# Kernel optimization log

Measured on AMD Instinct MI355X. Metric: run time of the kernel, lower is better.

## Reference

```python
import jax, jax.numpy as jnp
import numpy as np

NUM_USERS = 100000
NUM_MOVIES = 50000
NUM_NODES = NUM_USERS + NUM_MOVIES
EMB_DIM = 64
N_LAYERS = 3
N_EDGES = 4000000


def setup_inputs() -> dict:
    key = jax.random.key(0)
    k_e, k_w = jax.random.split(key)
    edge_index = jax.random.randint(k_e, (2, N_EDGES), 0, NUM_NODES, dtype=jnp.int64 if jax.config.jax_enable_x64 else jnp.int32)
    emb_weight = jax.random.normal(k_w, (NUM_NODES, EMB_DIM), dtype=jnp.float32)
    return {"edge_index": edge_index, "emb_weight": emb_weight}


def reference(edge_index, emb_weight):
    row, col = edge_index[0], edge_index[1]
    num_nodes = emb_weight.shape[0]
    # degree of each node as a scatter-add destination (col)
    deg = jax.ops.segment_sum(jnp.ones_like(col, dtype=emb_weight.dtype), col,
                              num_segments=num_nodes)
    deg_inv_sqrt = jnp.where(deg > 0, jax.lax.rsqrt(jnp.maximum(deg, 1.0)), 0.0)
    deg_inv_sqrt = jnp.where(deg > 0, deg ** -0.5, 0.0)
    norm = deg_inv_sqrt[row] * deg_inv_sqrt[col]  # [E]

    embs = emb_weight
    acc = emb_weight  # running sum for the final mean over layers
    for _ in range(N_LAYERS):
        msgs = norm[:, None] * embs[row]  # [E, D] gather + scale
        embs = jax.ops.segment_sum(msgs, col, num_segments=num_nodes)  # [N, D]
        acc = acc + embs
    return acc / (N_LAYERS + 1)
```

## Files before the change

### kernel.cpp

```cpp
#include <hip/hip_runtime.h>
#include <hip/hip_fp16.h>

#define D 64
constexpr int TPB = 256;
constexpr int PTPB = 1024;
constexpr int CTPB = 1024;
constexpr int VSHIFT = 8;
constexpr int VNODES = 1 << VSHIFT;
constexpr int CHUNK = 16384;
constexpr int CAP = 8192;
constexpr int MAXBUK = 640;
constexpr int GPAD = 16;
typedef unsigned short u16;

__device__ inline unsigned h2pack(float a, float b) {
    unsigned lo = __half_as_ushort(__float2half_rn(a));
    unsigned hi = __half_as_ushort(__float2half_rn(b));
    return lo | (hi << 16);
}

__global__ void fuseAB_kernel(const int* __restrict__ row, const int* __restrict__ col,
                              int* __restrict__ gcnt, unsigned* __restrict__ tmp,
                              int E, int NBUK) {
    __shared__ unsigned s_stage[CHUNK];
    __shared__ int h[MAXBUK];
    __shared__ int s[1024];
    __shared__ int gbase[MAXBUK];
    int t = threadIdx.x, blk = blockIdx.x;
    for (int b = t; b < MAXBUK; b += PTPB) h[b] = 0;
    __syncthreads();
    int base = blk * CHUNK;
    int n = min(CHUNK, E - base);
    for (int i = t; i < n; i += PTPB)
        atomicAdd(&h[col[base + i] >> VSHIFT], 1);
    __syncthreads();
    int v = (t < NBUK) ? h[t] : 0;
    if (t < NBUK && v > 0) gbase[t] = atomicAdd(&gcnt[t * GPAD], v);
    s[t] = v;
    __syncthreads();
    for (int off = 1; off < 1024; off <<= 1) {
        int x = (t >= off) ? s[t - off] : 0;
        __syncthreads();
        s[t] += x;
        __syncthreads();
    }
    s[t] -= v;
    __syncthreads();
    for (int i = t; i < n; i += PTPB) {
        int c = col[base + i];
        int b = c >> VSHIFT;
        int p = atomicAdd(&s[b], 1);
        s_stage[p] = ((unsigned)(c & (VNODES - 1)) << 18) | (unsigned)row[base + i];
    }
    __syncthreads();
    int w = t >> 6, lane = t & 63;
    for (int b = w; b < NBUK; b += (PTPB >> 6)) {
        int cnt = h[b];
        if (cnt == 0) continue;
        int lo = s[b] - cnt;
        int gb = gbase[b];
        unsigned* __restrict__ dst = tmp + (size_t)b * CAP;
        for (int j = lane; j < cnt; j += 64) {
            int p = gb + j;
            if (p < CAP)
                dst[p] = s_stage[lo + j];
        }
    }
}

__global__ void bscan_kernel(const int* __restrict__ gcnt, int* __restrict__ bExcl, int nb) {
    __shared__ int s[1024];
    int t = threadIdx.x;
    int v = (t < nb) ? gcnt[t * GPAD] : 0;
    s[t] = v;
    __syncthreads();
    for (int off = 1; off < 1024; off <<= 1) {
        int x = (t >= off) ? s[t - off] : 0;
        __syncthreads();
        s[t] += x;
        __syncthreads();
    }
    if (t < nb) bExcl[t] = s[t] - v;
}

__global__ void passC_kernel(const unsigned* __restrict__ tmp, const int* __restrict__ gcnt,
                             const int* __restrict__ bExcl,
                             int* __restrict__ row_ptr, float* __restrict__ dis,
                             int* __restrict__ srow,
                             const float2* __restrict__ emb2, unsigned* __restrict__ A,
                             int N, int E) {
    __shared__ int cnt[VNODES], sc[VNODES], cur[VNODES];
    int b = blockIdx.x, t = threadIdx.x;
    int nodeBase = b << VSHIFT;
    if (t < VNODES) cnt[t] = 0;
    if (b == 0 && t < 32) A[(size_t)N * 32 + t] = 0;
    __syncthreads();
    int m = min(gcnt[b * GPAD], CAP);
    const unsigned* __restrict__ tb = tmp + (size_t)b * CAP;
    for (int i = t; i < m; i += CTPB)
        atomicAdd(&cnt[tb[i] >> 18], 1);
    __syncthreads();
    if (t < VNODES) sc[t] = cnt[t];
    __syncthreads();
    for (int off = 1; off < VNODES; off <<= 1) {
        int i = (t + 1) * (off << 1) - 1;
        if (i < VNODES) sc[i] += sc[i - off];
        __syncthreads();
    }
    if (t == 0) sc[VNODES - 1] = 0;
    __syncthreads();
    for (int off = VNODES / 2; off >= 1; off >>= 1) {
        int i = (t + 1) * (off << 1) - 1;
        if (i < VNODES) { int x = sc[i - off]; sc[i - off] = sc[i]; sc[i] += x; }
        __syncthreads();
    }
    int gbase = bExcl[b];
    if (t < VNODES) {
        int rp = gbase + sc[t];
        cur[t] = rp;
        int node = nodeBase + t;
        if (node < N) {
            row_ptr[node] = rp;
            int d = cnt[t];
            dis[node] = (d > 0) ? rsqrtf((float)d) : 0.0f;
        }
    }
    if (b == 0 && t == 0) row_ptr[N] = E;
    __syncthreads();
    for (int i = t; i < m; i += CTPB) {
        unsigned pk = tb[i];
        int p = atomicAdd(&cur[pk >> 18], 1);
        srow[p] = (int)(pk & 0x3FFFFu);
    }
    for (int i = t; i < (VNODES << 5); i += CTPB) {
        int k = i >> 5;
        int node = nodeBase + k;
        if (node < N) {
            int d = cnt[k];
            float dv = (d > 0) ? rsqrtf((float)d) : 0.0f;
            size_t o = (size_t)node * 32 + (i & 31);
            float2 x = emb2[o];
            A[o] = h2pack(dv * x.x, dv * x.y);
        }
    }
}

#define ACC8(u) do { \
    a0 += __half2float(__ushort_as_half((u16)((u).x & 0xffff))); \
    a1 += __half2float(__ushort_as_half((u16)((u).x >> 16)));    \
    a2 += __half2float(__ushort_as_half((u16)((u).y & 0xffff))); \
    a3 += __half2float(__ushort_as_half((u16)((u).y >> 16)));    \
    a4 += __half2float(__ushort_as_half((u16)((u).z & 0xffff))); \
    a5 += __half2float(__ushort_as_half((u16)((u).z >> 16)));    \
    a6 += __half2float(__ushort_as_half((u16)((u).w & 0xffff))); \
    a7 += __half2float(__ushort_as_half((u16)((u).w >> 16)));    \
} while (0)

template <int MODE, bool WRITE_DST>
__global__ void spmm_kernel(const int* __restrict__ row_ptr, const int* __restrict__ srow,
                            const float* __restrict__ dis,
                            const unsigned* __restrict__ src, unsigned* __restrict__ dst,
                            float2* __restrict__ out2, const float2* __restrict__ emb2,
                            int N) {
    if (WRITE_DST && blockIdx.x == 0 && threadIdx.x < 32)
        dst[(size_t)N * 32 + threadIdx.x] = 0;
    int wave = (blockIdx.x * blockDim.x + threadIdx.x) >> 6;
    int lane = threadIdx.x & 63;
    int half = lane >> 5;
    int sub  = lane & 31;
    int node = 2 * wave + half;
    if (node >= N) return;
    int start = row_ptr[node];
    int end   = row_ptr[node + 1];
    int hb = half << 5;
    int rg = sub >> 3;
    int q  = sub & 7;
    const uint4* __restrict__ s4 = (const uint4*)src;
    float a0 = 0, a1 = 0, a2 = 0, a3 = 0, a4 = 0, a5 = 0, a6 = 0, a7 = 0;
    for (int base = start; base < end; base += 32) {
        int mye = base + sub;
        int rr = (mye < end) ? srow[mye] : 0;
        int cnt = end - base;
        int r0 = __shfl(rr, hb +  0 + rg);
        int r1 = __shfl(rr, hb +  4 + rg);
        int r2 = __shfl(rr, hb +  8 + rg);
        int r3 = __shfl(rr, hb + 12 + rg);
        int r4 = __shfl(rr, hb + 16 + rg);
        int r5 = __shfl(rr, hb + 20 + rg);
        int r6 = __shfl(rr, hb + 24 + rg);
        int r7 = __shfl(rr, hb + 28 + rg);
        r0 = ( 0 + rg < cnt) ? r0 : N;
        r1 = ( 4 + rg < cnt) ? r1 : N;
        r2 = ( 8 + rg < cnt) ? r2 : N;
        r3 = (12 + rg < cnt) ? r3 : N;
        r4 = (16 + rg < cnt) ? r4 : N;
        r5 = (20 + rg < cnt) ? r5 : N;
        r6 = (24 + rg < cnt) ? r6 : N;
        r7 = (28 + rg < cnt) ? r7 : N;
        uint4 u0 = s4[(size_t)r0 * 8 + q];
        uint4 u1 = s4[(size_t)r1 * 8 + q];
        uint4 u2 = s4[(size_t)r2 * 8 + q];
        uint4 u3 = s4[(size_t)r3 * 8 + q];
        uint4 u4 = s4[(size_t)r4 * 8 + q];
        uint4 u5 = s4[(size_t)r5 * 8 + q];
        uint4 u6 = s4[(size_t)r6 * 8 + q];
        uint4 u7 = s4[(size_t)r7 * 8 + q];
        ACC8(u0); ACC8(u1); ACC8(u2); ACC8(u3);
        ACC8(u4); ACC8(u5); ACC8(u6); ACC8(u7);
    }
    a0 += __shfl_xor(a0, 8);  a1 += __shfl_xor(a1, 8);
    a2 += __shfl_xor(a2, 8);  a3 += __shfl_xor(a3, 8);
    a4 += __shfl_xor(a4, 8);  a5 += __shfl_xor(a5, 8);
    a6 += __shfl_xor(a6, 8);  a7 += __shfl_xor(a7, 8);
    a0 += __shfl_xor(a0, 16); a1 += __shfl_xor(a1, 16);
    a2 += __shfl_xor(a2, 16); a3 += __shfl_xor(a3, 16);
    a4 += __shfl_xor(a4, 16); a5 += __shfl_xor(a5, 16);
    a6 += __shfl_xor(a6, 16); a7 += __shfl_xor(a7, 16);
    if (rg != 0) return;
    float dc = dis[node];
    float e0 = dc * a0, e1 = dc * a1, e2 = dc * a2, e3 = dc * a3;
    float e4 = dc * a4, e5 = dc * a5, e6 = dc * a6, e7 = dc * a7;
    if (WRITE_DST) {
        uint4 pk;
        pk.x = h2pack(dc * e0, dc * e1);
        pk.y = h2pack(dc * e2, dc * e3);
        pk.z = h2pack(dc * e4, dc * e5);
        pk.w = h2pack(dc * e6, dc * e7);
        ((uint4*)dst)[(size_t)node * 8 + q] = pk;
    }
    size_t fo = (size_t)node * 16 + q * 2;
    float4* __restrict__ o4 = (float4*)out2;
    float4 c0, c1;
    if (MODE == 0) {
        const float4* __restrict__ e4p = (const float4*)emb2;
        c0 = e4p[fo]; c1 = e4p[fo + 1];
        c0.x += e0; c0.y += e1; c0.z += e2; c0.w += e3;
        c1.x += e4; c1.y += e5; c1.z += e6; c1.w += e7;
    } else if (MODE == 1) {
        c0 = o4[fo]; c1 = o4[fo + 1];
        c0.x += e0; c0.y += e1; c0.z += e2; c0.w += e3;
        c1.x += e4; c1.y += e5; c1.z += e6; c1.w += e7;
    } else {
        c0 = o4[fo]; c1 = o4[fo + 1];
        c0.x = (c0.x + e0) * 0.25f; c0.y = (c0.y + e1) * 0.25f;
        c0.z = (c0.z + e2) * 0.25f; c0.w = (c0.w + e3) * 0.25f;
        c1.x = (c1.x + e4) * 0.25f; c1.y = (c1.y + e5) * 0.25f;
        c1.z = (c1.z + e6) * 0.25f; c1.w = (c1.w + e7) * 0.25f;
    }
    o4[fo] = c0; o4[fo + 1] = c1;
}

extern "C" void kernel_launch(void* const* d_in, const int* in_sizes, int n_in,
                              void* d_out, int out_size, void* d_ws, size_t ws_size,
                              hipStream_t stream) {
    const int* edge = (const int*)d_in[0];
    const float* emb = (const float*)d_in[1];
    const int E = in_sizes[0] / 2;
    const int N = in_sizes[1] / D;
    float2* out2 = (float2*)d_out;

    const int* row = edge;
    const int* col = edge + E;

    const int NBLK = (E + CHUNK - 1) / CHUNK;
    const int NBUK = (N + VNODES - 1) >> VSHIFT;

    size_t zrow = (size_t)(N + 1) * 32;
    size_t tsz  = (size_t)NBUK * CAP;
    size_t bsz  = (tsz > zrow) ? tsz : zrow;
    unsigned* A       = (unsigned*)d_ws;
    unsigned* B       = A + zrow;
    unsigned* tmp     = B;
    int*      srow    = (int*)(B + bsz);
    int*      row_ptr = srow + E;
    float*    dis     = (float*)(row_ptr + N + 1);
    int*      gcnt    = (int*)(dis + N);
    int*      bExcl   = gcnt + NBUK * GPAD;

    const int spmm_blocks = (((N + 1) / 2) * 64 + TPB - 1) / TPB;

    hipMemsetAsync(gcnt, 0, (size_t)NBUK * GPAD * sizeof(int), stream);
    fuseAB_kernel<<<NBLK, PTPB, 0, stream>>>(row, col, gcnt, tmp, E, NBUK);
    bscan_kernel<<<1, 1024, 0, stream>>>(gcnt, bExcl, NBUK);
    passC_kernel<<<NBUK, CTPB, 0, stream>>>(tmp, gcnt, bExcl, row_ptr, dis,
                                            srow, (const float2*)emb, A, N, E);

    spmm_kernel<0, true><<<spmm_blocks, TPB, 0, stream>>>(row_ptr, srow, dis, A, B,
                                                          out2, (const float2*)emb, N);
    spmm_kernel<1, true><<<spmm_blocks, TPB, 0, stream>>>(row_ptr, srow, dis, B, A,
                                                          out2, (const float2*)emb, N);
    spmm_kernel<2, false><<<spmm_blocks, TPB, 0, stream>>>(row_ptr, srow, dis, A, nullptr,
                                                           out2, (const float2*)emb, N);
}
```

Baseline: 414.5 us.

## Stage CSR column writes in LDS and rebuild final output from fp16 layer buffers

passC now scatters each bucket's source indices into a shared-memory buffer first, then writes them to global srow in one contiguous, coalesced pass instead of scattering them straight to global memory. The first two SpMM layers no longer read-modify-write the fp32 output accumulator; they only write the fp16 scaled embedding buffers. The final layer rebuilds the layer-1 and layer-2 contributions from those fp16 buffers, unscaling by 1/dis. This removes two full fp32 output round trips, at the cost of fp16 rounding on those contributions and 32KB of extra LDS per passC block.

After: 378.2 us. 1.1x faster.

```diff
diff --git a/kernel.cpp b/kernel.cpp
--- a/kernel.cpp
+++ b/kernel.cpp
@@ -90,6 +90,7 @@
                              const float2* __restrict__ emb2, unsigned* __restrict__ A,
                              int N, int E) {
     __shared__ int cnt[VNODES], sc[VNODES], cur[VNODES];
+    __shared__ int s_out[CAP];
     int b = blockIdx.x, t = threadIdx.x;
     int nodeBase = b << VSHIFT;
     if (t < VNODES) cnt[t] = 0;
@@ -116,11 +117,10 @@
     }
     int gbase = bExcl[b];
     if (t < VNODES) {
-        int rp = gbase + sc[t];
-        cur[t] = rp;
+        cur[t] = sc[t];
         int node = nodeBase + t;
         if (node < N) {
-            row_ptr[node] = rp;
+            row_ptr[node] = gbase + sc[t];
             int d = cnt[t];
             dis[node] = (d > 0) ? rsqrtf((float)d) : 0.0f;
         }
@@ -130,8 +130,11 @@
     for (int i = t; i < m; i += CTPB) {
         unsigned pk = tb[i];
         int p = atomicAdd(&cur[pk >> 18], 1);
-        srow[p] = (int)(pk & 0x3FFFFu);
-    }
+        s_out[p] = (int)(pk & 0x3FFFFu);
+    }
+    __syncthreads();
+    for (int i = t; i < m; i += CTPB)
+        srow[gbase + i] = s_out[i];
     for (int i = t; i < (VNODES << 5); i += CTPB) {
         int k = i >> 5;
         int node = nodeBase + k;
@@ -155,11 +158,14 @@
     a6 += __half2float(__ushort_as_half((u16)((u).w & 0xffff))); \
     a7 += __half2float(__ushort_as_half((u16)((u).w >> 16)));    \
 } while (0)
+#define UHLO(u) __half2float(__ushort_as_half((u16)((u) & 0xffff)))
+#define UHHI(u) __half2float(__ushort_as_half((u16)((u) >> 16)))
 
 template <int MODE, bool WRITE_DST>
 __global__ void spmm_kernel(const int* __restrict__ row_ptr, const int* __restrict__ srow,
                             const float* __restrict__ dis,
                             const unsigned* __restrict__ src, unsigned* __restrict__ dst,
+                            const unsigned* __restrict__ other,
                             float2* __restrict__ out2, const float2* __restrict__ emb2,
                             int N) {
     if (WRITE_DST && blockIdx.x == 0 && threadIdx.x < 32)
@@ -228,26 +234,24 @@
         pk.w = h2pack(dc * e6, dc * e7);
         ((uint4*)dst)[(size_t)node * 8 + q] = pk;
     }
-    size_t fo = (size_t)node * 16 + q * 2;
-    float4* __restrict__ o4 = (float4*)out2;
-    float4 c0, c1;
-    if (MODE == 0) {
+    if (MODE == 2) {
+        float inv = (dc > 0.0f) ? 1.0f / dc : 0.0f;
+        uint4 za = ((const uint4*)src)[(size_t)node * 8 + q];
+        uint4 zb = ((const uint4*)other)[(size_t)node * 8 + q];
+        size_t fo = (size_t)node * 16 + q * 2;
         const float4* __restrict__ e4p = (const float4*)emb2;
-        c0 = e4p[fo]; c1 = e4p[fo + 1];
-        c0.x += e0; c0.y += e1; c0.z += e2; c0.w += e3;
-        c1.x += e4; c1.y += e5; c1.z += e6; c1.w += e7;
-    } else if (MODE == 1) {
-        c0 = o4[fo]; c1 = o4[fo + 1];
-        c0.x += e0; c0.y += e1; c0.z += e2; c0.w += e3;
-        c1.x += e4; c1.y += e5; c1.z += e6; c1.w += e7;
-    } else {
-        c0 = o4[fo]; c1 = o4[fo + 1];
-        c0.x = (c0.x + e0) * 0.25f; c0.y = (c0.y + e1) * 0.25f;
-        c0.z = (c0.z + e2) * 0.25f; c0.w = (c0.w + e3) * 0.25f;
-        c1.x = (c1.x + e4) * 0.25f; c1.y = (c1.y + e5) * 0.25f;
-        c1.z = (c1.z + e6) * 0.25f; c1.w = (c1.w + e7) * 0.25f;
-    }
-    o4[fo] = c0; o4[fo + 1] = c1;
+        float4 c0 = e4p[fo], c1 = e4p[fo + 1];
+        c0.x = 0.25f * (c0.x + inv * (UHLO(za.x) + UHLO(zb.x)) + e0);
+        c0.y = 0.25f * (c0.y + inv * (UHHI(za.x) + UHHI(zb.x)) + e1);
+        c0.z = 0.25f * (c0.z + inv * (UHLO(za.y) + UHLO(zb.y)) + e2);
+        c0.w = 0.25f * (c0.w + inv * (UHHI(za.y) + UHHI(zb.y)) + e3);
+        c1.x = 0.25f * (c1.x + inv * (UHLO(za.z) + UHLO(zb.z)) + e4);
+        c1.y = 0.25f * (c1.y + inv * (UHHI(za.z) + UHHI(zb.z)) + e5);
+        c1.z = 0.25f * (c1.z + inv * (UHLO(za.w) + UHLO(zb.w)) + e6);
+        c1.w = 0.25f * (c1.w + inv * (UHHI(za.w) + UHHI(zb.w)) + e7);
+        float4* __restrict__ o4 = (float4*)out2;
+        o4[fo] = c0; o4[fo + 1] = c1;
+    }
 }
 
 extern "C" void kernel_launch(void* const* d_in, const int* in_sizes, int n_in,
@@ -286,9 +290,12 @@
                                             srow, (const float2*)emb, A, N, E);
 
     spmm_kernel<0, true><<<spmm_blocks, TPB, 0, stream>>>(row_ptr, srow, dis, A, B,
-                                                          out2, (const float2*)emb, N);
-    spmm_kernel<1, true><<<spmm_blocks, TPB, 0, stream>>>(row_ptr, srow, dis, B, A,
-                                                          out2, (const float2*)emb, N);
+                                                          nullptr, out2,
+                                                          (const float2*)emb, N);
+    spmm_kernel<0, true><<<spmm_blocks, TPB, 0, stream>>>(row_ptr, srow, dis, B, A,
+                                                          nullptr, out2,
+                                                          (const float2*)emb, N);
     spmm_kernel<2, false><<<spmm_blocks, TPB, 0, stream>>>(row_ptr, srow, dis, A, nullptr,
-                                                           out2, (const float2*)emb, N);
-}
+                                                           B, out2,
+                                                           (const float2*)emb, N);
+}
```
